# Kernel optimization log

Hardware: AMD Instinct MI355X
Metric: run time of the kernel (lower is better)

The kernel has to match this reference:

```python
import jax, jax.numpy as jnp
import numpy as np

B, L, D = 8, 1024, 1024  # L must equal D for the elementwise sqrt(K) divide to broadcast


def setup_inputs() -> dict:
    key = jax.random.key(0)
    ks = jax.random.split(key, 9)
    # Non-negative inputs/weights/biases so K = x @ Wk.T + bk >= 0 and sqrt(K) is finite.
    rc = jax.random.uniform(ks[0], (B, L, D), dtype=jnp.float32)
    ri = jax.random.uniform(ks[1], (B, L, D), dtype=jnp.float32)
    tc = jax.random.uniform(ks[2], (B, L, D), dtype=jnp.float32)
    scale = 0.02
    Wq = jax.random.uniform(ks[3], (D, D), dtype=jnp.float32) * scale
    Wk = jax.random.uniform(ks[4], (D, D), dtype=jnp.float32) * scale
    Wv = jax.random.uniform(ks[5], (D, D), dtype=jnp.float32) * scale
    bq = jax.random.uniform(ks[6], (D,), dtype=jnp.float32) * scale
    bk = jax.random.uniform(ks[7], (D,), dtype=jnp.float32) * scale
    bv = jax.random.uniform(ks[8], (D,), dtype=jnp.float32) * scale
    return {
        "reference_caption": rc,
        "reference_image": ri,
        "target_caption": tc,
        "Wq": Wq, "bq": bq,
        "Wk": Wk, "bk": bk,
        "Wv": Wv, "bv": bv,
    }


def reference(reference_caption, reference_image, target_caption, Wq, bq, Wk, bk, Wv, bv):
    # torch nn.Linear: y = x @ W.T + b
    Q = reference_caption @ Wq.T + bq          # [B, Lq, D]
    K = reference_image @ Wk.T + bk            # [B, Lk, D]
    V = reference_image @ Wv.T + bv            # [B, Lk, D]
    matmul_qk = jnp.einsum("bqd,bkd->bqk", Q, K)  # [B, Lq, Lk]
    # Faithful to source: elementwise divide by sqrt(K) tensor (broadcasts since Lq==Lk==D).
    scaled_logits = matmul_qk / jnp.sqrt(K)
    attention_weights = jax.nn.softmax(scaled_logits, axis=-1)
    output = jnp.einsum("bqk,bkd->bqd", attention_weights, V)
    return (output, attention_weights)
```

## Files before the change

kernel.cpp:

```cpp
#include <hip/hip_runtime.h>
#include <hip/hip_fp16.h>
#include <math.h>

typedef unsigned short u16;
typedef __attribute__((ext_vector_type(8))) _Float16 half8;
typedef __attribute__((ext_vector_type(4))) float f32x4;

#define ASLOT 4096
#define SLOT  12288

__device__ __forceinline__ u16 f2h(float f){ __half h=__float2half(f); u16 r; __builtin_memcpy(&r,&h,2); return r; }
__device__ __forceinline__ float h2f(u16 u){ __half h; __builtin_memcpy(&h,&u,2); return __half2float(h); }

template<int ROWS>
__device__ __forceinline__ void stage_tile(const u16* __restrict__ G, int rowbase, int ldg,
                                           int k0, u16* Ls, int tid){
#pragma unroll
    for (int p = 0; p < ROWS / 64; ++p){
        const int lin = tid + p * 256;
        const int row = lin >> 2;
        const int cg  = ((lin & 3) ^ ((row >> 1) & 3)) * 8;
        const u16* g = G + (size_t)(rowbase + row) * ldg + (k0 + cg);
        __builtin_amdgcn_global_load_lds(
            (__attribute__((address_space(1))) void*)g,
            (__attribute__((address_space(3))) void*)(Ls + (size_t)lin * 8), 16, 0, 0);
    }
}

template<int EPI, int BIASM>
__device__ __forceinline__ void gemm_core(
    const u16* __restrict__ A, const u16* __restrict__ B,
    const float* __restrict__ bias,
    float* __restrict__ of, u16* __restrict__ oh,
    const float* __restrict__ cm, u16* __restrict__ od,
    int by, int bx, int lda, int ldb, int ldc, int K, u16* sh)
{
    const int tid  = threadIdx.x;
    const int lane = tid & 63, wv = tid >> 6;
    const int wr = (wv >> 1) * 64;
    const int wc = (wv & 1) * 128;
    const int row0 = by * 128, col0 = bx * 256;
    const int lr = lane & 15, hi = lane >> 4;
    const int co = (hi ^ ((lr >> 1) & 3)) * 8;

    f32x4 acc[4][8];
#pragma unroll
    for (int m = 0; m < 4; m++)
#pragma unroll
        for (int n = 0; n < 8; n++) acc[m][n] = (f32x4){0.f, 0.f, 0.f, 0.f};

    auto stage_set = [&](int buf, int k0){
        u16* s = sh + buf * SLOT;
        stage_tile<128>(A, row0, lda, k0, s, tid);
        stage_tile<256>(B, col0, ldb, k0, s + ASLOT, tid);
    };

    const int NIT = K >> 5;
    stage_set(0, 0);
    stage_set(1, 32);
    int bufs = 2, bufr = 0;
    for (int t = 0; t < NIT; ++t){
        if (t + 2 < NIT){ stage_set(bufs, (t + 2) << 5); bufs = (bufs + 1 == 3) ? 0 : bufs + 1; }
        const int rem = NIT - 1 - t;
        if (rem >= 2)      asm volatile("s_waitcnt vmcnt(12)" ::: "memory");
        else if (rem == 1) asm volatile("s_waitcnt vmcnt(6)" ::: "memory");
        else               asm volatile("s_waitcnt vmcnt(0)" ::: "memory");
        __builtin_amdgcn_s_barrier();
        __builtin_amdgcn_sched_barrier(0);

        const u16* s = sh + bufr * SLOT;
        bufr = (bufr + 1 == 3) ? 0 : bufr + 1;

        half8 a[4], b[8];
#pragma unroll
        for (int m = 0; m < 4; m++) a[m] = *(const half8*)&s[(wr + m * 16 + lr) * 32 + co];
#pragma unroll
        for (int n = 0; n < 8; n++) b[n] = *(const half8*)&s[ASLOT + (wc + n * 16 + lr) * 32 + co];
#pragma unroll
        for (int m = 0; m < 4; m++)
#pragma unroll
            for (int n = 0; n < 8; n++)
                acc[m][n] = __builtin_amdgcn_mfma_f32_16x16x32_f16(a[m], b[n], acc[m][n], 0, 0, 0);
        __builtin_amdgcn_sched_barrier(0);
        __builtin_amdgcn_s_barrier();
    }

#pragma unroll
    for (int m = 0; m < 4; m++) {
        const int rb = row0 + wr + m * 16 + hi * 4;
#pragma unroll
        for (int n = 0; n < 8; n++) {
            const int c = col0 + wc + n * 16 + lr;
            const float bc = (BIASM == 1) ? bias[c] : 0.f;
#pragma unroll
            for (int q = 0; q < 4; q++) {
                const int r = rb + q;
                float v = acc[m][n][q] + bc;
                if (BIASM == 2) v += bias[r];
                const size_t idx = (size_t)r * ldc + c;
                if (EPI == 0) of[idx] = v;
                else if (EPI == 1) oh[idx] = f2h(v);
                else {
                    const float d  = v - cm[(size_t)((r >> 10) << 10) + c];
                    const u16  dh = f2h(d);
                    oh[idx] = dh;
                    od[idx] = f2h(d - h2f(dh));
                }
            }
        }
    }
}

__global__ __launch_bounds__(256, 2) void tri_k(
    const u16* __restrict__ rc_h, const u16* __restrict__ ri_h,
    const u16* __restrict__ Wq_h, const u16* __restrict__ Wk_h,
    const u16* __restrict__ Wv_h,
    const float* __restrict__ bq, const float* __restrict__ bk,
    const float* __restrict__ bv, const float* __restrict__ cm,
    u16* __restrict__ Q_h, u16* __restrict__ Kd, u16* __restrict__ Krs,
    u16* __restrict__ Vt)
{
    __shared__ __align__(16) u16 sh[3 * SLOT];
    const int nwg = gridDim.x, chunk = nwg >> 3;
    const int swz = ((int)blockIdx.x & 7) * chunk + ((int)blockIdx.x >> 3);
    const int p = swz % 3, t = swz / 3;
    if (p == 0) {
        gemm_core<1, 1>(rc_h, Wq_h, bq, nullptr, Q_h, nullptr, nullptr,
                        t >> 2, t & 3, 1024, 1024, 1024, 1024, sh);
    } else if (p == 1) {
        gemm_core<5, 1>(ri_h, Wk_h, bk, nullptr, Kd, cm, Krs,
                        t >> 2, t & 3, 1024, 1024, 1024, 1024, sh);
    } else {
        gemm_core<1, 2>(Wv_h, ri_h, bv, nullptr, Vt, nullptr, nullptr,
                        t >> 5, t & 31, 1024, 1024, 8192, 1024, sh);
    }
}

__global__ __launch_bounds__(256, 2) void qkt_k(
    const u16* __restrict__ Q_h, const u16* __restrict__ Kd,
    const float* __restrict__ u, float* __restrict__ wts)
{
    __shared__ __align__(16) u16 sh[3 * SLOT];
    const int nwg = gridDim.x, chunk = nwg >> 3;
    const int swz = ((int)blockIdx.x & 7) * chunk + ((int)blockIdx.x >> 3);
    const int z = swz >> 5, rem = swz & 31;
    gemm_core<0, 2>(Q_h + ((size_t)z << 20), Kd + ((size_t)z << 20),
                    u + ((size_t)z << 10), wts + ((size_t)z << 20), nullptr,
                    nullptr, nullptr,
                    rem >> 2, rem & 3, 1024, 1024, 1024, 1024, sh);
}

__global__ __launch_bounds__(256, 2) void av_k(
    const u16* __restrict__ W_h, const u16* __restrict__ Vt, float* __restrict__ outp)
{
    __shared__ __align__(16) u16 sh[3 * SLOT];
    const int nwg = gridDim.x, chunk = nwg >> 3;
    const int wg = ((int)blockIdx.x & 7) * chunk + ((int)blockIdx.x >> 3);
    const int z = wg >> 5, rem = wg & 31;
    gemm_core<0, 0>(W_h + ((size_t)z << 20), Vt + (size_t)z * 1024,
                    nullptr, outp + ((size_t)z << 20), nullptr, nullptr, nullptr,
                    rem >> 2, rem & 3, 1024, 8192, 1024, 1024, sh);
}

__global__ __launch_bounds__(256)
void colmean_k(const u16* __restrict__ ri_h, float* __restrict__ xbar)
{
    const int b = blockIdx.x >> 5, sub = blockIdx.x & 31;
    const int dg = sub & 3, rg = sub >> 2;
    const int d = dg * 256 + threadIdx.x;
    const u16* base = ri_h + ((size_t)b << 20) + ((size_t)(rg * 128) << 10) + d;
    float s = 0.f;
#pragma unroll 4
    for (int r = 0; r < 128; ++r) s += h2f(base[(size_t)r << 10]);
    atomicAdd(&xbar[(b << 10) + d], s * (1.f / 1024.f));
}

template<bool BIAS, bool AFULL>
__global__ __launch_bounds__(256)
void rowdot_k(const u16* __restrict__ A, const float* __restrict__ B,
              const float* __restrict__ bias, float* __restrict__ out)
{
    const int o = blockIdx.x * 4 + (threadIdx.x >> 6);
    const int lane = threadIdx.x & 63;
    const int ar = AFULL ? o : (o & 1023);
    const int br = o >> 10;
    const u16* ap = A + ((size_t)ar << 10);
    const float* bp = B + ((size_t)br << 10);
    float s = 0.f;
#pragma unroll
    for (int j = 0; j < 16; ++j){ const int i = lane + (j << 6); s += h2f(ap[i]) * bp[i]; }
#pragma unroll
    for (int off = 32; off >= 1; off >>= 1) s += __shfl_xor(s, off);
    if (lane == 0) out[o] = s + (BIAS ? bias[ar] : 0.f);
}

__global__ __launch_bounds__(256)
void softmax_scale_k(float* __restrict__ W, const u16* __restrict__ Kd,
                     const u16* __restrict__ Krs, const float* __restrict__ cm,
                     u16* __restrict__ Wh)
{
    const long row = blockIdx.x;
    const int b = (int)(row >> 10);
    float* p = W + (row << 10);
    const int tid = threadIdx.x;

    float4 v = ((const float4*)p)[tid];
    const ushort4 kd = ((const ushort4*)(Kd + (row << 10)))[tid];
    const ushort4 ks = ((const ushort4*)(Krs + (row << 10)))[tid];
    const float4 cmv = ((const float4*)(cm + ((size_t)b << 10)))[tid];
    v.x *= rsqrtf(h2f(kd.x) + h2f(ks.x) + cmv.x);
    v.y *= rsqrtf(h2f(kd.y) + h2f(ks.y) + cmv.y);
    v.z *= rsqrtf(h2f(kd.z) + h2f(ks.z) + cmv.z);
    v.w *= rsqrtf(h2f(kd.w) + h2f(ks.w) + cmv.w);

    float m = fmaxf(fmaxf(v.x, v.y), fmaxf(v.z, v.w));
#pragma unroll
    for (int o = 32; o >= 1; o >>= 1) m = fmaxf(m, __shfl_xor(m, o));
    __shared__ float sm[4];
    const int wid = tid >> 6, lane = tid & 63;
    if (lane == 0) sm[wid] = m;
    __syncthreads();
    m = fmaxf(fmaxf(sm[0], sm[1]), fmaxf(sm[2], sm[3]));

    v.x = __expf(v.x - m); v.y = __expf(v.y - m);
    v.z = __expf(v.z - m); v.w = __expf(v.w - m);
    float s = v.x + v.y + v.z + v.w;
#pragma unroll
    for (int o = 32; o >= 1; o >>= 1) s += __shfl_xor(s, o);
    __shared__ float ss[4];
    if (lane == 0) ss[wid] = s;
    __syncthreads();
    s = ss[0] + ss[1] + ss[2] + ss[3];

    const float inv = 1.0f / s;
    v.x *= inv; v.y *= inv; v.z *= inv; v.w *= inv;
    ((float4*)p)[tid] = v;

    ushort4 ub;
    ub.x = f2h(v.x); ub.y = f2h(v.y); ub.z = f2h(v.z); ub.w = f2h(v.w);
    ((ushort4*)(Wh + (row << 10)))[tid] = ub;
}

__global__ __launch_bounds__(256)
void conv_plain5_k(const float4* __restrict__ x0, ushort4* __restrict__ y0,
                   const float4* __restrict__ x1, ushort4* __restrict__ y1,
                   const float4* __restrict__ x2, ushort4* __restrict__ y2,
                   const float4* __restrict__ x3, ushort4* __restrict__ y3,
                   const float4* __restrict__ x4, ushort4* __restrict__ y4)
{
    const long i = (long)blockIdx.x * 256 + threadIdx.x;
    const long n0 = 2097152, n1 = 262144;
    const float4* x; ushort4* y; long j;
    if (i < n0)                 { x = x0; y = y0; j = i; }
    else if (i < 2*n0)          { x = x1; y = y1; j = i - n0; }
    else if (i < 2*n0 + n1)     { x = x2; y = y2; j = i - 2*n0; }
    else if (i < 2*n0 + 2*n1)   { x = x3; y = y3; j = i - 2*n0 - n1; }
    else                        { x = x4; y = y4; j = i - 2*n0 - 2*n1; }
    const float4 v = x[j];
    ushort4 o;
    o.x = f2h(v.x); o.y = f2h(v.y); o.z = f2h(v.z); o.w = f2h(v.w);
    y[j] = o;
}

extern "C" void kernel_launch(void* const* d_in, const int* in_sizes, int n_in,
                              void* d_out, int out_size, void* d_ws, size_t ws_size,
                              hipStream_t stream)
{
    const float* rc = (const float*)d_in[0];
    const float* ri = (const float*)d_in[1];
    const float* Wq = (const float*)d_in[3];
    const float* bq = (const float*)d_in[4];
    const float* Wk = (const float*)d_in[5];
    const float* bk = (const float*)d_in[6];
    const float* Wv = (const float*)d_in[7];
    const float* bv = (const float*)d_in[8];

    const long M8 = 8192 * 1024L;
    const long M1 = 1024 * 1024L;

    u16* ws   = (u16*)d_ws;
    u16* ri_h = ws;
    u16* rc_h = ws + 1 * M8;
    u16* Kd   = ws + 2 * M8;
    u16* Krs  = ws + 3 * M8;
    u16* Vt   = ws + 4 * M8;
    u16* Wq_h = ws + 5 * M8;
    u16* Wk_h = Wq_h + M1;
    u16* Wv_h = Wk_h + M1;
    float* xbar = (float*)(ws + 5 * M8 + 3 * M1);
    float* cm   = xbar + 8192;
    float* uu   = cm + 8192;

    float* outp = (float*)d_out;
    float* wts  = outp + M8;
    u16*   Q_h  = (u16*)d_out;
    u16*   W_h  = ri_h;

    conv_plain5_k<<<19456, 256, 0, stream>>>(
        (const float4*)ri, (ushort4*)ri_h, (const float4*)rc, (ushort4*)rc_h,
        (const float4*)Wq, (ushort4*)Wq_h, (const float4*)Wk, (ushort4*)Wk_h,
        (const float4*)Wv, (ushort4*)Wv_h);

    hipMemsetAsync(xbar, 0, 8192 * sizeof(float), stream);
    colmean_k<<<256, 256, 0, stream>>>(ri_h, xbar);

    rowdot_k<true, false><<<2048, 256, 0, stream>>>(Wk_h, xbar, bk, cm);

    tri_k<<<768, 256, 0, stream>>>(rc_h, ri_h, Wq_h, Wk_h, Wv_h,
                                   bq, bk, bv, cm, Q_h, Kd, Krs, Vt);

    rowdot_k<false, true><<<2048, 256, 0, stream>>>(Q_h, cm, nullptr, uu);

    qkt_k<<<256, 256, 0, stream>>>(Q_h, Kd, uu, wts);

    softmax_scale_k<<<8192, 256, 0, stream>>>(wts, Kd, Krs, cm, W_h);

    av_k<<<256, 256, 0, stream>>>(W_h, Vt, outp);
}
```

Measured before the change: 174.4 us.

## Move V projection GEMM into the QK^T launch to balance grids

The fused Q/K/V projection launch of 768 workgroups is split. Q and K projections now run in a 512-workgroup kernel. The V-transpose projection is merged with the QK^T logits GEMM into a second 512-workgroup kernel. This makes the two launches more even and fills the previously undersized 256-workgroup QK^T launch. Vt now reuses the rc_h workspace buffer, which is dead after the Q projection, and frees one large workspace slot.

New measurement: 166.4 us. -4.6%, faster.

```diff
diff --git a/kernel.cpp b/kernel.cpp
--- a/kernel.cpp
+++ b/kernel.cpp
@@ -111,43 +111,46 @@
     }
 }
 
-__global__ __launch_bounds__(256, 2) void tri_k(
+__global__ __launch_bounds__(256, 2) void lin_qk_k(
     const u16* __restrict__ rc_h, const u16* __restrict__ ri_h,
     const u16* __restrict__ Wq_h, const u16* __restrict__ Wk_h,
-    const u16* __restrict__ Wv_h,
     const float* __restrict__ bq, const float* __restrict__ bk,
-    const float* __restrict__ bv, const float* __restrict__ cm,
-    u16* __restrict__ Q_h, u16* __restrict__ Kd, u16* __restrict__ Krs,
-    u16* __restrict__ Vt)
+    const float* __restrict__ cm,
+    u16* __restrict__ Q_h, u16* __restrict__ Kd, u16* __restrict__ Krs)
 {
     __shared__ __align__(16) u16 sh[3 * SLOT];
     const int nwg = gridDim.x, chunk = nwg >> 3;
     const int swz = ((int)blockIdx.x & 7) * chunk + ((int)blockIdx.x >> 3);
-    const int p = swz % 3, t = swz / 3;
+    const int p = swz & 1, t = swz >> 1;
     if (p == 0) {
         gemm_core<1, 1>(rc_h, Wq_h, bq, nullptr, Q_h, nullptr, nullptr,
                         t >> 2, t & 3, 1024, 1024, 1024, 1024, sh);
-    } else if (p == 1) {
+    } else {
         gemm_core<5, 1>(ri_h, Wk_h, bk, nullptr, Kd, cm, Krs,
                         t >> 2, t & 3, 1024, 1024, 1024, 1024, sh);
+    }
+}
+
+__global__ __launch_bounds__(256, 2) void qkt_vt_k(
+    const u16* __restrict__ Q_h, const u16* __restrict__ Kd,
+    const u16* __restrict__ ri_h, const u16* __restrict__ Wv_h,
+    const float* __restrict__ bv, const float* __restrict__ u,
+    float* __restrict__ wts, u16* __restrict__ Vt)
+{
+    __shared__ __align__(16) u16 sh[3 * SLOT];
+    const int nwg = gridDim.x, chunk = nwg >> 3;
+    const int swz = ((int)blockIdx.x & 7) * chunk + ((int)blockIdx.x >> 3);
+    const int p = swz & 1, t = swz >> 1;
+    if (p == 0) {
+        const int z = t >> 5, rem = t & 31;
+        gemm_core<0, 2>(Q_h + ((size_t)z << 20), Kd + ((size_t)z << 20),
+                        u + ((size_t)z << 10), wts + ((size_t)z << 20), nullptr,
+                        nullptr, nullptr,
+                        rem >> 2, rem & 3, 1024, 1024, 1024, 1024, sh);
     } else {
         gemm_core<1, 2>(Wv_h, ri_h, bv, nullptr, Vt, nullptr, nullptr,
                         t >> 5, t & 31, 1024, 1024, 8192, 1024, sh);
     }
-}
-
-__global__ __launch_bounds__(256, 2) void qkt_k(
-    const u16* __restrict__ Q_h, const u16* __restrict__ Kd,
-    const float* __restrict__ u, float* __restrict__ wts)
-{
-    __shared__ __align__(16) u16 sh[3 * SLOT];
-    const int nwg = gridDim.x, chunk = nwg >> 3;
-    const int swz = ((int)blockIdx.x & 7) * chunk + ((int)blockIdx.x >> 3);
-    const int z = swz >> 5, rem = swz & 31;
-    gemm_core<0, 2>(Q_h + ((size_t)z << 20), Kd + ((size_t)z << 20),
-                    u + ((size_t)z << 10), wts + ((size_t)z << 20), nullptr,
-                    nullptr, nullptr,
-                    rem >> 2, rem & 3, 1024, 1024, 1024, 1024, sh);
 }
 
 __global__ __launch_bounds__(256, 2) void av_k(
@@ -283,17 +286,17 @@
     u16* rc_h = ws + 1 * M8;
     u16* Kd   = ws + 2 * M8;
     u16* Krs  = ws + 3 * M8;
-    u16* Vt   = ws + 4 * M8;
-    u16* Wq_h = ws + 5 * M8;
+    u16* Wq_h = ws + 4 * M8;
     u16* Wk_h = Wq_h + M1;
     u16* Wv_h = Wk_h + M1;
-    float* xbar = (float*)(ws + 5 * M8 + 3 * M1);
+    float* xbar = (float*)(ws + 4 * M8 + 3 * M1);
     float* cm   = xbar + 8192;
     float* uu   = cm + 8192;
 
     float* outp = (float*)d_out;
     float* wts  = outp + M8;
     u16*   Q_h  = (u16*)d_out;
+    u16*   Vt   = rc_h;
     u16*   W_h  = ri_h;
 
     conv_plain5_k<<<19456, 256, 0, stream>>>(
@@ -306,12 +309,11 @@
 
     rowdot_k<true, false><<<2048, 256, 0, stream>>>(Wk_h, xbar, bk, cm);
 
-    tri_k<<<768, 256, 0, stream>>>(rc_h, ri_h, Wq_h, Wk_h, Wv_h,
-                                   bq, bk, bv, cm, Q_h, Kd, Krs, Vt);
+    lin_qk_k<<<512, 256, 0, stream>>>(rc_h, ri_h, Wq_h, Wk_h, bq, bk, cm, Q_h, Kd, Krs);
 
     rowdot_k<false, true><<<2048, 256, 0, stream>>>(Q_h, cm, nullptr, uu);
 
-    qkt_k<<<256, 256, 0, stream>>>(Q_h, Kd, uu, wts);
+    qkt_vt_k<<<512, 256, 0, stream>>>(Q_h, Kd, ri_h, Wv_h, bv, uu, wts, Vt);
 
     softmax_scale_k<<<8192, 256, 0, stream>>>(wts, Kd, Krs, cm, W_h);
 
```
